# Kernel tuning notes

Hardware: AMD Instinct MI355X
Metric: run time of the kernel (lower is better)

## Reference

```python
import jax, jax.numpy as jnp
import numpy as np

HEATMAPS_LOSS_FACTOR = 1.0
PUSH_LOSS_FACTOR = 0.001
PULL_LOSS_FACTOR = 0.001

B, K, H, W, M = 16, 17, 256, 256, 30  # batch, joints, heatmap HxW, max people
N = K * H * W  # flattened tag length per image


def setup_inputs() -> dict:
    key = jax.random.key(0)
    k1, k2, k3, k4, k5, k6 = jax.random.split(key, 6)
    heatmaps_pred = jax.random.normal(k1, (B, K, H, W), dtype=jnp.float32)
    heatmaps = jax.random.uniform(k2, (B, K, H, W), dtype=jnp.float32)
    masks = (jax.random.uniform(k3, (B, K, H, W)) > 0.1).astype(jnp.float32)
    tags_pred = jax.random.normal(k4, (B, K, H, W), dtype=jnp.float32)
    idx = jax.random.randint(k5, (B, M, K), 0, N)
    vis = jax.random.randint(k6, (B, M, K), 0, 2)  # ~half joints visible
    joints = jnp.stack([idx, vis], axis=-1).astype(jnp.int32)
    return {
        "heatmaps_pred": heatmaps_pred,
        "heatmaps": heatmaps,
        "masks": masks,
        "tags_pred": tags_pred,
        "joints": joints,
    }


def _single_tag_loss(tag_flat, joints_img):
    # tag_flat: [N], joints_img: [M, K, 2] (flat index, visibility)
    idx = joints_img[..., 0]                      # [M, K]
    vis = (joints_img[..., 1] > 0)                # [M, K] bool
    visf = vis.astype(tag_flat.dtype)
    t = tag_flat[idx]                             # [M, K] gathered tags
    cnt = jnp.sum(visf, axis=-1)                  # [M] visible joints per person
    person_valid = cnt > 0                        # [M]
    safe_cnt = jnp.maximum(cnt, 1.0)
    mu = jnp.sum(t * visf, axis=-1) / safe_cnt    # [M] per-person mean tag
    pull_pp = jnp.sum(visf * (t - mu[:, None]) ** 2, axis=-1) / safe_cnt  # [M]
    n = jnp.sum(person_valid.astype(tag_flat.dtype))  # num_tags
    pull = jnp.sum(jnp.where(person_valid, pull_pp, 0.0)) / jnp.maximum(n, 1.0)
    # push: pairwise exp(-(mu_i - mu_j)^2) over valid persons; diagonal sums to n
    diff = mu[:, None] - mu[None, :]              # [M, M]
    pair_mask = person_valid[:, None] & person_valid[None, :]
    s = jnp.sum(jnp.where(pair_mask, jnp.exp(-(diff ** 2)), 0.0))
    denom = jnp.maximum((n - 1.0) * n, 1.0)
    push = jnp.where(n >= 2.0, (s - n) / denom * 0.5, 0.0)
    return push, pull


def reference(heatmaps_pred, heatmaps, masks, tags_pred, joints):
    # HeatmapLoss: mean over all dims of (pred - gt)^2 * mask
    heatmaps_loss = jnp.mean((heatmaps_pred - heatmaps) ** 2 * masks)
    heatmaps_loss = heatmaps_loss * HEATMAPS_LOSS_FACTOR
    # AELoss over flattened tag maps, vectorized across the batch
    b = tags_pred.shape[0]
    tag_flat = tags_pred.reshape(b, -1)           # [B, N]
    push, pull = jax.vmap(_single_tag_loss)(tag_flat, joints)
    push_loss = jnp.mean(push) * PUSH_LOSS_FACTOR
    pull_loss = jnp.mean(pull) * PULL_LOSS_FACTOR
    return (heatmaps_loss, push_loss, pull_loss)
```

## Files before the change

### kernel.cpp

```cpp
#include <hip/hip_runtime.h>

#define Bn 16
#define Kn 17
#define Hn 256
#define Wn 256
#define Mn 30
#define NFLAT (Kn * Hn * Wn)
#define TOTAL ((long long)Bn * Kn * Hn * Wn)
#define NVEC  ((int)(TOTAL / 4))
#define NPAIR (NVEC / 2)

#define HEAT_BLOCKS 2048
#define THREADS 256
#define AE_BLOCKS Bn

__global__ __launch_bounds__(THREADS) void fused_kernel(
    const float4* __restrict__ pred,
    const float4* __restrict__ gt,
    const float4* __restrict__ mask,
    const float* __restrict__ tags,
    const int* __restrict__ joints,
    float* __restrict__ partial,
    float* __restrict__ push_arr,
    float* __restrict__ pull_arr) {
    __shared__ float smem[64];

    if (blockIdx.x < HEAT_BLOCKS) {
        int tid = blockIdx.x * THREADS + threadIdx.x;
        const int stride = HEAT_BLOCKS * THREADS;
        float acc0 = 0.f, acc1 = 0.f;
        for (int i = tid; i < NPAIR; i += stride) {
            float4 p0 = pred[2 * i], p1 = pred[2 * i + 1];
            float4 g0 = gt[2 * i],   g1 = gt[2 * i + 1];
            float4 m0 = mask[2 * i], m1 = mask[2 * i + 1];
            float dx, dy, dz, dw;
            dx = p0.x - g0.x; dy = p0.y - g0.y; dz = p0.z - g0.z; dw = p0.w - g0.w;
            acc0 += dx * dx * m0.x + dy * dy * m0.y + dz * dz * m0.z + dw * dw * m0.w;
            dx = p1.x - g1.x; dy = p1.y - g1.y; dz = p1.z - g1.z; dw = p1.w - g1.w;
            acc1 += dx * dx * m1.x + dy * dy * m1.y + dz * dz * m1.z + dw * dw * m1.w;
        }
        float a = acc0 + acc1;
        for (int off = 32; off > 0; off >>= 1) a += __shfl_down(a, off, 64);
        int wave = threadIdx.x >> 6;
        if ((threadIdx.x & 63) == 0) smem[wave] = a;
        __syncthreads();
        if (threadIdx.x == 0)
            partial[blockIdx.x] = smem[0] + smem[1] + smem[2] + smem[3];
    } else {
        int b = blockIdx.x - HEAT_BLOCKS;
        int lane = threadIdx.x;

        float mu = 0.f, pullpp = 0.f, validf = 0.f;
        if (lane < Mn) {
            const int* jb = joints + ((long long)(b * Mn + lane) * Kn) * 2;
            const float* tb = tags + (long long)b * NFLAT;
            float t[Kn], v[Kn];
            float cnt = 0.f, st = 0.f;
#pragma unroll
            for (int k = 0; k < Kn; k++) {
                int id = jb[2 * k];
                int vi = jb[2 * k + 1];
                float tv = tb[id];
                t[k] = tv;
                v[k] = (vi > 0) ? 1.f : 0.f;
                cnt += v[k];
                st += v[k] * tv;
            }
            float sc = fmaxf(cnt, 1.f);
            mu = st / sc;
            float pp = 0.f;
#pragma unroll
            for (int k = 0; k < Kn; k++) {
                float d = t[k] - mu;
                pp += v[k] * d * d;
            }
            pullpp = pp / sc;
            validf = (cnt > 0.f) ? 1.f : 0.f;
            smem[lane] = mu;
            smem[32 + lane] = validf;
        }
        __syncthreads();

        if (lane < 64) {
            float nv = validf;
            float pv = (validf > 0.f) ? pullpp : 0.f;
            float sm = 0.f;
            if (lane < Mn && validf > 0.f) {
                for (int j = 0; j < Mn; j++) {
                    if (smem[32 + j] > 0.f) {
                        float d = mu - smem[j];
                        sm += expf(-(d * d));
                    }
                }
            }
            for (int off = 32; off > 0; off >>= 1) {
                nv += __shfl_down(nv, off, 64);
                pv += __shfl_down(pv, off, 64);
                sm += __shfl_down(sm, off, 64);
            }
            if (lane == 0) {
                float n = nv;
                float pull = pv / fmaxf(n, 1.f);
                float denom = fmaxf((n - 1.f) * n, 1.f);
                float push = (n >= 2.f) ? (sm - n) / denom * 0.5f : 0.f;
                out_push:
                push_arr[b] = push;
                pull_arr[b] = pull;
            }
        }
    }
}

__global__ __launch_bounds__(256) void finalize_kernel(
    const float* __restrict__ partial, int nblocks,
    const float* __restrict__ push_arr,
    const float* __restrict__ pull_arr,
    float* __restrict__ out) {
    __shared__ double sd[256];
    double acc = 0.0;
    for (int i = threadIdx.x; i < nblocks; i += 256) acc += (double)partial[i];
    sd[threadIdx.x] = acc;
    __syncthreads();
    for (int off = 128; off > 0; off >>= 1) {
        if (threadIdx.x < off) sd[threadIdx.x] += sd[threadIdx.x + off];
        __syncthreads();
    }
    if (threadIdx.x == 0) {
        double heat = sd[0] / (double)TOTAL;
        float psum = 0.f, lsum = 0.f;
        for (int b = 0; b < Bn; b++) {
            psum += push_arr[b];
            lsum += pull_arr[b];
        }
        out[0] = (float)heat;
        out[1] = (psum / (float)Bn) * 0.001f;
        out[2] = (lsum / (float)Bn) * 0.001f;
    }
}

extern "C" void kernel_launch(void* const* d_in, const int* in_sizes, int n_in,
                              void* d_out, int out_size, void* d_ws, size_t ws_size,
                              hipStream_t stream) {
    const float* heatmaps_pred = (const float*)d_in[0];
    const float* heatmaps      = (const float*)d_in[1];
    const float* masks         = (const float*)d_in[2];
    const float* tags_pred     = (const float*)d_in[3];
    const int*   joints        = (const int*)d_in[4];
    float* out = (float*)d_out;

    float* ws = (float*)d_ws;
    float* partial  = ws;
    float* push_arr = ws + HEAT_BLOCKS;
    float* pull_arr = push_arr + Bn;

    fused_kernel<<<HEAT_BLOCKS + AE_BLOCKS, THREADS, 0, stream>>>(
        (const float4*)heatmaps_pred, (const float4*)heatmaps,
        (const float4*)masks, tags_pred, joints, partial, push_arr, pull_arr);

    finalize_kernel<<<1, 256, 0, stream>>>(partial, HEAT_BLOCKS,
                                           push_arr, pull_arr, out);
}
```

Measured before the change: 40.84 us.

## Fuse finalize into main kernel via last-block atomic ticket; fixed-trip heat loop

Removes the separate finalize kernel launch: each block takes an atomic ticket after a threadfence, and the last block to finish does the final double-precision reduction and writes the outputs. The counter is zeroed with a memset on the stream before launch. The heatmap grid becomes 2176 blocks that each handle exactly 8 float4 per thread in a fully unrolled loop, so all loads can be in flight at once. In exchange it adds a memset operation, per-block atomic and fence overhead, and a serial tail reduction inside the last block.

```diff
diff --git a/kernel.cpp b/kernel.cpp
--- a/kernel.cpp
+++ b/kernel.cpp
@@ -8,11 +8,16 @@
 #define NFLAT (Kn * Hn * Wn)
 #define TOTAL ((long long)Bn * Kn * Hn * Wn)
 #define NVEC  ((int)(TOTAL / 4))
-#define NPAIR (NVEC / 2)
 
-#define HEAT_BLOCKS 2048
+#define HEAT_BLOCKS 2176
 #define THREADS 256
+#define PER_THREAD 8
 #define AE_BLOCKS Bn
+#define NBLOCKS (HEAT_BLOCKS + AE_BLOCKS)
+
+#define WS_PARTIAL 64
+#define WS_PUSH (WS_PARTIAL + HEAT_BLOCKS)
+#define WS_PULL (WS_PUSH + Bn)
 
 __global__ __launch_bounds__(THREADS) void fused_kernel(
     const float4* __restrict__ pred,
@@ -20,29 +25,32 @@
     const float4* __restrict__ mask,
     const float* __restrict__ tags,
     const int* __restrict__ joints,
-    float* __restrict__ partial,
-    float* __restrict__ push_arr,
-    float* __restrict__ pull_arr) {
+    float* __restrict__ ws,
+    float* __restrict__ out) {
     __shared__ float smem[64];
+    __shared__ int is_last;
+
+    unsigned int* counter = (unsigned int*)ws;
+    float* partial  = ws + WS_PARTIAL;
+    float* push_arr = ws + WS_PUSH;
+    float* pull_arr = ws + WS_PULL;
 
     if (blockIdx.x < HEAT_BLOCKS) {
-        int tid = blockIdx.x * THREADS + threadIdx.x;
+        int t = blockIdx.x * THREADS + threadIdx.x;
         const int stride = HEAT_BLOCKS * THREADS;
-        float acc0 = 0.f, acc1 = 0.f;
-        for (int i = tid; i < NPAIR; i += stride) {
-            float4 p0 = pred[2 * i], p1 = pred[2 * i + 1];
-            float4 g0 = gt[2 * i],   g1 = gt[2 * i + 1];
-            float4 m0 = mask[2 * i], m1 = mask[2 * i + 1];
-            float dx, dy, dz, dw;
-            dx = p0.x - g0.x; dy = p0.y - g0.y; dz = p0.z - g0.z; dw = p0.w - g0.w;
-            acc0 += dx * dx * m0.x + dy * dy * m0.y + dz * dz * m0.z + dw * dw * m0.w;
-            dx = p1.x - g1.x; dy = p1.y - g1.y; dz = p1.z - g1.z; dw = p1.w - g1.w;
-            acc1 += dx * dx * m1.x + dy * dy * m1.y + dz * dz * m1.z + dw * dw * m1.w;
+        float acc = 0.f;
+#pragma unroll
+        for (int u = 0; u < PER_THREAD; ++u) {
+            int i = u * stride + t;
+            float4 p = pred[i];
+            float4 g = gt[i];
+            float4 m = mask[i];
+            float dx = p.x - g.x, dy = p.y - g.y, dz = p.z - g.z, dw = p.w - g.w;
+            acc += dx * dx * m.x + dy * dy * m.y + dz * dz * m.z + dw * dw * m.w;
         }
-        float a = acc0 + acc1;
-        for (int off = 32; off > 0; off >>= 1) a += __shfl_down(a, off, 64);
+        for (int off = 32; off > 0; off >>= 1) acc += __shfl_down(acc, off, 64);
         int wave = threadIdx.x >> 6;
-        if ((threadIdx.x & 63) == 0) smem[wave] = a;
+        if ((threadIdx.x & 63) == 0) smem[wave] = acc;
         __syncthreads();
         if (threadIdx.x == 0)
             partial[blockIdx.x] = smem[0] + smem[1] + smem[2] + smem[3];
@@ -103,38 +111,41 @@
                 float pull = pv / fmaxf(n, 1.f);
                 float denom = fmaxf((n - 1.f) * n, 1.f);
                 float push = (n >= 2.f) ? (sm - n) / denom * 0.5f : 0.f;
-                out_push:
                 push_arr[b] = push;
                 pull_arr[b] = pull;
             }
         }
     }
-}
 
-__global__ __launch_bounds__(256) void finalize_kernel(
-    const float* __restrict__ partial, int nblocks,
-    const float* __restrict__ push_arr,
-    const float* __restrict__ pull_arr,
-    float* __restrict__ out) {
-    __shared__ double sd[256];
-    double acc = 0.0;
-    for (int i = threadIdx.x; i < nblocks; i += 256) acc += (double)partial[i];
-    sd[threadIdx.x] = acc;
+    if (threadIdx.x == 0) {
+        __threadfence();
+        unsigned int ticket = atomicAdd(counter, 1u);
+        is_last = (ticket == (unsigned int)(NBLOCKS - 1)) ? 1 : 0;
+    }
     __syncthreads();
-    for (int off = 128; off > 0; off >>= 1) {
-        if (threadIdx.x < off) sd[threadIdx.x] += sd[threadIdx.x + off];
+    if (is_last) {
+        __threadfence();
+        __shared__ double sd[THREADS];
+        double acc = 0.0;
+        for (int i = threadIdx.x; i < HEAT_BLOCKS; i += THREADS)
+            acc += (double)partial[i];
+        sd[threadIdx.x] = acc;
         __syncthreads();
-    }
-    if (threadIdx.x == 0) {
-        double heat = sd[0] / (double)TOTAL;
-        float psum = 0.f, lsum = 0.f;
-        for (int b = 0; b < Bn; b++) {
-            psum += push_arr[b];
-            lsum += pull_arr[b];
+        for (int off = THREADS / 2; off > 0; off >>= 1) {
+            if (threadIdx.x < off) sd[threadIdx.x] += sd[threadIdx.x + off];
+            __syncthreads();
         }
-        out[0] = (float)heat;
-        out[1] = (psum / (float)Bn) * 0.001f;
-        out[2] = (lsum / (float)Bn) * 0.001f;
+        if (threadIdx.x == 0) {
+            double heat = sd[0] / (double)TOTAL;
+            float psum = 0.f, lsum = 0.f;
+            for (int b = 0; b < Bn; b++) {
+                psum += push_arr[b];
+                lsum += pull_arr[b];
+            }
+            out[0] = (float)heat;
+            out[1] = (psum / (float)Bn) * 0.001f;
+            out[2] = (lsum / (float)Bn) * 0.001f;
+        }
     }
 }
 
@@ -147,16 +158,11 @@
     const float* tags_pred     = (const float*)d_in[3];
     const int*   joints        = (const int*)d_in[4];
     float* out = (float*)d_out;
+    float* ws  = (float*)d_ws;
 
-    float* ws = (float*)d_ws;
-    float* partial  = ws;
-    float* push_arr = ws + HEAT_BLOCKS;
-    float* pull_arr = push_arr + Bn;
+    hipMemsetAsync(d_ws, 0, sizeof(unsigned int), stream);
 
-    fused_kernel<<<HEAT_BLOCKS + AE_BLOCKS, THREADS, 0, stream>>>(
+    fused_kernel<<<NBLOCKS, THREADS, 0, stream>>>(
         (const float4*)heatmaps_pred, (const float4*)heatmaps,
-        (const float4*)masks, tags_pred, joints, partial, push_arr, pull_arr);
-
-    finalize_kernel<<<1, 256, 0, stream>>>(partial, HEAT_BLOCKS,
-                                           push_arr, pull_arr, out);
+        (const float4*)masks, tags_pred, joints, ws, out);
 }
```

New measurement: 114.3 us. 180% more time.
